# Optimization experiments

Hardware: AMD Instinct MI355X
Metric: run time of the kernel (lower is better)

The kernel has to match this reference:

```python
import jax, jax.numpy as jnp
import numpy as np

N_LOC = 20000
N_EXP = 200000
H = 64
E = 1500000
L = 400000


def setup_inputs() -> dict:
    key = jax.random.key(0)
    ks = jax.random.split(key, 24)
    f = jnp.float32
    w = lambda k, shp: jax.random.normal(k, shp, dtype=f) * 0.1
    # edges: ('location','of','experts'): src in [0,N_LOC), dst in [0,N_EXP)
    src = jax.random.randint(ks[0], (E,), 0, N_LOC)
    dst = jax.random.randint(ks[1], (E,), 0, N_EXP)
    edge_of = jnp.stack([src, dst])          # location -> experts
    edge_rev = jnp.stack([dst, src])         # experts -> location (ToUndirected)
    row = jax.random.randint(ks[2], (L,), 0, N_LOC)
    col = jax.random.randint(ks[3], (L,), 0, N_EXP)
    edge_label_index = jnp.stack([row, col])
    return dict(
        emb_loc=w(ks[4], (N_LOC, H)), emb_exp=w(ks[5], (N_EXP, H)),
        W1l_of=w(ks[6], (H, H)), b1_of=jnp.zeros((H,), f), W1r_of=w(ks[7], (H, H)),
        W1l_rev=w(ks[8], (H, H)), b1_rev=jnp.zeros((H,), f), W1r_rev=w(ks[9], (H, H)),
        W2l_of=w(ks[10], (H, H)), b2_of=jnp.zeros((H,), f), W2r_of=w(ks[11], (H, H)),
        W2l_rev=w(ks[12], (H, H)), b2_rev=jnp.zeros((H,), f), W2r_rev=w(ks[13], (H, H)),
        dW1=w(ks[14], (2 * H, H)), db1=jnp.zeros((H,), f),
        dW2=w(ks[15], (H, 1)), db2=jnp.zeros((1,), f),
        edge_of=edge_of, edge_rev=edge_rev, edge_label_index=edge_label_index,
    )


def _sage(x_src, x_dst, edge, Wl, b, Wr, n_dst):
    # PyG SAGEConv: lin_l(mean of neighbor msgs) + lin_r(x_dst); bias only in lin_l
    s, d = edge[0], edge[1]
    msg = x_src[s]                                   # [E, H] gather
    summed = jax.ops.segment_sum(msg, d, num_segments=n_dst)
    cnt = jax.ops.segment_sum(jnp.ones((edge.shape[1],), x_src.dtype), d, num_segments=n_dst)
    agg = summed / jnp.maximum(cnt, 1.0)[:, None]
    return agg @ Wl + b + x_dst @ Wr


def reference(emb_loc, emb_exp,
              W1l_of, b1_of, W1r_of, W1l_rev, b1_rev, W1r_rev,
              W2l_of, b2_of, W2r_of, W2l_rev, b2_rev, W2r_rev,
              dW1, db1, dW2, db2,
              edge_of, edge_rev, edge_label_index):
    # layer 1 (to_hetero: one conv per edge type; each dst type has one incoming type)
    z_exp = jax.nn.relu(_sage(emb_loc, emb_exp, edge_of, W1l_of, b1_of, W1r_of, N_EXP))
    z_loc = jax.nn.relu(_sage(emb_exp, emb_loc, edge_rev, W1l_rev, b1_rev, W1r_rev, N_LOC))
    # layer 2 (no relu)
    z_exp2 = _sage(z_loc, z_exp, edge_of, W2l_of, b2_of, W2r_of, N_EXP)
    z_loc2 = _sage(z_exp, z_loc, edge_rev, W2l_rev, b2_rev, W2r_rev, N_LOC)
    # EdgeDecoder: gather-concat-MLP
    row, col = edge_label_index[0], edge_label_index[1]
    z = jnp.concatenate([z_loc2[row], z_exp2[col]], axis=-1)  # [L, 2H]
    h = jax.nn.relu(z @ dW1 + db1)
    out = (h @ dW2 + db2).reshape(-1)
    return out
```

## Files before the change

kernel.cpp:

```cpp
#include <hip/hip_runtime.h>

#define H 64
#define NE 1500000
#define NLOC 20000
#define NEXP 200000
#define NL 400000
#define PAD_E 32
#define PAD_L 128
#define EPT 8
#define FILL_CHUNK 2048
#define NCHUNK ((NE + FILL_CHUNK - 1) / FILL_CHUNK)

#define WS_NEED 90546112ULL

typedef int vint4 __attribute__((ext_vector_type(4)));
typedef _Float16 f16x8 __attribute__((ext_vector_type(8)));
typedef float f32x4 __attribute__((ext_vector_type(4)));

__device__ __forceinline__ float bcastf(float v, int k) {
  return __int_as_float(__builtin_amdgcn_readlane(__float_as_int(v), k));
}
__device__ __forceinline__ int bcasti(int v, int k) {
  return __builtin_amdgcn_readlane(v, k);
}

__global__ __launch_bounds__(256) void fill_kernel(
    const int* __restrict__ src, const int* __restrict__ dst,
    int* __restrict__ cnt_loc, int* __restrict__ cnt_exp,
    int* __restrict__ nbr_loc, unsigned short* __restrict__ nbr_exp)
{
  const int p = blockIdx.x & 7;
  const int chunk = blockIdx.x >> 3;
  const long base = (long)chunk * FILL_CHUNK + threadIdx.x * EPT;
  if (base >= NE) return;
  vint4 s0 = __builtin_nontemporal_load((const vint4*)(src + base));
  vint4 s1 = __builtin_nontemporal_load((const vint4*)(src + base + 4));
  vint4 d0 = __builtin_nontemporal_load((const vint4*)(dst + base));
  vint4 d1 = __builtin_nontemporal_load((const vint4*)(dst + base + 4));
  int ss[EPT] = {s0.x, s0.y, s0.z, s0.w, s1.x, s1.y, s1.z, s1.w};
  int dd[EPT] = {d0.x, d0.y, d0.z, d0.w, d1.x, d1.y, d1.z, d1.w};
  const int elo = p * (NEXP / 8), ehi = elo + NEXP / 8;
  const int llo = p * (NLOC / 8), lhi = llo + NLOC / 8;
#pragma unroll
  for (int k = 0; k < EPT; k++) {
    const int d = dd[k];
    if (d >= elo && d < ehi) {
      int pos = atomicAdd(&cnt_exp[d], 1);
      if (pos < PAD_E) nbr_exp[d * PAD_E + pos] = (unsigned short)ss[k];
    }
  }
#pragma unroll
  for (int k = 0; k < EPT; k++) {
    const int s = ss[k];
    if (s >= llo && s < lhi) {
      int pos = atomicAdd(&cnt_loc[s], 1);
      if (pos < PAD_L) nbr_loc[s * PAD_L + pos] = dd[k];
    }
  }
}

__global__ __launch_bounds__(256) void fold_kernel(
    const float* __restrict__ W2r_of, const float* __restrict__ W2l_of,
    const float* __restrict__ W2l_rev, const float* __restrict__ W2r_rev,
    const float* __restrict__ dW1, const float* __restrict__ b2_of,
    const float* __restrict__ b2_rev,
    float* __restrict__ Wf_q, float* __restrict__ Wf_y2,
    float* __restrict__ Wf_t2, float* __restrict__ Wf_p,
    float* __restrict__ bf_q, float* __restrict__ bf_p)
{
  const int lane = threadIdx.x & 63;
  const int w = threadIdx.x >> 6;
  const float* dW1a = dW1;
  const float* dW1b = dW1 + H * H;
  if (blockIdx.x < 4) {
    const float* A; const float* B; float* C;
    switch (blockIdx.x) {
      case 0:  A = W2r_of;  B = dW1b; C = Wf_q;  break;
      case 1:  A = W2l_of;  B = dW1b; C = Wf_y2; break;
      case 2:  A = W2l_rev; B = dW1a; C = Wf_t2; break;
      default: A = W2r_rev; B = dW1a; C = Wf_p;  break;
    }
    float b[H];
#pragma unroll
    for (int k = 0; k < H; k++) b[k] = B[k * H + lane];
    for (int r = w * 16; r < w * 16 + 16; r++) {
      const float xv = A[r * H + lane];
      float a0 = 0.f, a1 = 0.f;
#pragma unroll
      for (int k = 0; k < H; k += 2) {
        a0 += bcastf(xv, k)     * b[k];
        a1 += bcastf(xv, k + 1) * b[k + 1];
      }
      C[r * H + lane] = a0 + a1;
    }
  } else if (w < 2) {
    const float* bv_src = (w == 0) ? b2_of : b2_rev;
    const float* B      = (w == 0) ? dW1b  : dW1a;
    float* o            = (w == 0) ? bf_q  : bf_p;
    float wk[H];
#pragma unroll
    for (int k = 0; k < H; k++) wk[k] = B[k * H + lane];
    const float bv = bv_src[lane];
    float a = 0.f;
#pragma unroll
    for (int k = 0; k < H; k++) a += bcastf(bv, k) * wk[k];
    o[lane] = a;
  }
}

__global__ __launch_bounds__(256, 4) void dense_linear_kernel(
    const float* __restrict__ x, _Float16* __restrict__ out16,
    const float* __restrict__ W, int n)
{
  const int lane = threadIdx.x & 63;
  const int gw = (blockIdx.x * 256 + threadIdx.x) >> 6;
  const int nw = (gridDim.x * 256) >> 6;
  float w[H];
#pragma unroll
  for (int k = 0; k < H; k++) w[k] = W[k * H + lane];
  for (int i = gw; i < n; i += nw) {
    const float xv = x[i * H + lane];
    float a0 = 0.f, a1 = 0.f;
#pragma unroll
    for (int k = 0; k < H; k += 2) {
      a0 += bcastf(xv, k)     * w[k];
      a1 += bcastf(xv, k + 1) * w[k + 1];
    }
    out16[i * H + lane] = (_Float16)(a0 + a1);
  }
}

__global__ __launch_bounds__(256, 4) void mfma_pass_kernel(
    const unsigned short* __restrict__ nbr, const int* __restrict__ cnt,
    const _Float16* __restrict__ y,
    const float* a32, const _Float16* a16,
    _Float16* out1, const float* __restrict__ W1,
    const float* __restrict__ bias, int relu,
    _Float16* out2, const float* __restrict__ W2)
{
  const int w = threadIdx.x >> 6;
  const int lane = threadIdx.x & 63;
  const int q = lane >> 4;
  const int cidx = lane & 15;
  const int rb = blockIdx.x * 16;

  __shared__ float Gs[16 * H];

  f16x8 b1lo, b1hi, b2lo, b2hi;
#pragma unroll
  for (int j = 0; j < 8; j++) {
    b1lo[j] = (_Float16)W1[(q * 8 + j) * H + w * 16 + cidx];
    b1hi[j] = (_Float16)W1[(32 + q * 8 + j) * H + w * 16 + cidx];
  }
  if (out2) {
#pragma unroll
    for (int j = 0; j < 8; j++) {
      b2lo[j] = (_Float16)W2[(q * 8 + j) * H + w * 16 + cidx];
      b2hi[j] = (_Float16)W2[(32 + q * 8 + j) * H + w * 16 + cidx];
    }
  }

  if (y) {
    for (int rr = 0; rr < 4; rr++) {
      const int i = rb + w * 4 + rr;
      const int c = cnt[i];
      const int cc = min(c, PAD_E);
      const unsigned short* nb = nbr + (long)i * PAD_E;
      float s0 = 0.f, s1 = 0.f, s2 = 0.f, s3 = 0.f;
      const int id = (lane < cc) ? (int)nb[lane] : 0;
      int k = 0;
      const int m4 = cc & ~3;
      for (; k < m4; k += 4) {
        const int i0 = bcasti(id, k), i1 = bcasti(id, k + 1),
                  i2 = bcasti(id, k + 2), i3 = bcasti(id, k + 3);
        s0 += (float)y[(long)i0 * H + lane];
        s1 += (float)y[(long)i1 * H + lane];
        s2 += (float)y[(long)i2 * H + lane];
        s3 += (float)y[(long)i3 * H + lane];
      }
      for (; k < cc; k++) s0 += (float)y[(long)bcasti(id, k) * H + lane];
      Gs[(w * 4 + rr) * H + lane] =
          ((s0 + s1) + (s2 + s3)) / fmaxf((float)c, 1.0f);
    }
  }

  f16x8 a0, a1;
  if (a16) {
    const _Float16* ar = a16 + (long)(rb + cidx) * H;
    a0 = *(const f16x8*)(ar + q * 8);
    a1 = *(const f16x8*)(ar + 32 + q * 8);
  } else {
    const float* ar = a32 + (long)(rb + cidx) * H;
#pragma unroll
    for (int j = 0; j < 8; j++) {
      a0[j] = (_Float16)ar[q * 8 + j];
      a1[j] = (_Float16)ar[32 + q * 8 + j];
    }
  }
  f32x4 acc1 = {0.f, 0.f, 0.f, 0.f};
  acc1 = __builtin_amdgcn_mfma_f32_16x16x32_f16(a0, b1lo, acc1, 0, 0, 0);
  acc1 = __builtin_amdgcn_mfma_f32_16x16x32_f16(a1, b1hi, acc1, 0, 0, 0);
  f32x4 acc2 = {0.f, 0.f, 0.f, 0.f};
  if (out2) {
    acc2 = __builtin_amdgcn_mfma_f32_16x16x32_f16(a0, b2lo, acc2, 0, 0, 0);
    acc2 = __builtin_amdgcn_mfma_f32_16x16x32_f16(a1, b2hi, acc2, 0, 0, 0);
  }

  const float bj = bias ? bias[w * 16 + cidx] : 0.f;
  __syncthreads();
#pragma unroll
  for (int reg = 0; reg < 4; reg++) {
    const int r = q * 4 + reg;
    float v = acc1[reg] + bj;
    if (y) v += Gs[r * H + w * 16 + cidx];
    if (relu) v = fmaxf(v, 0.f);
    out1[(long)(rb + r) * H + w * 16 + cidx] = (_Float16)v;
    if (out2)
      out2[(long)(rb + r) * H + w * 16 + cidx] = (_Float16)acc2[reg];
  }
}

__global__ __launch_bounds__(256, 4) void loc_gather_kernel(
    const int* __restrict__ nbr, const int* __restrict__ cnt,
    const _Float16* __restrict__ T, const float* __restrict__ x,
    float* __restrict__ out32, _Float16* __restrict__ out16,
    const float* __restrict__ Wr, const float* __restrict__ bias,
    int n, int relu)
{
  const int lane = threadIdx.x & 63;
  const int gw = (blockIdx.x * 256 + threadIdx.x) >> 6;
  const int nw = (gridDim.x * 256) >> 6;
  float wr[H];
#pragma unroll
  for (int k = 0; k < H; k++) wr[k] = Wr[k * H + lane];
  const float bj = bias[lane];
  for (int i = gw; i < n; i += nw) {
    const int c = cnt[i];
    const int cc = min(c, PAD_L);
    const int* nb = nbr + (long)i * PAD_L;
    float s0 = 0.f, s1 = 0.f, s2 = 0.f, s3 = 0.f;
    int e = 0;
    while (e < cc) {
      const int m = min(cc - e, 64);
      const int id = (lane < m) ? nb[e + lane] : 0;
      int k = 0;
      const int m4 = m & ~3;
      for (; k < m4; k += 4) {
        const int i0 = bcasti(id, k), i1 = bcasti(id, k + 1),
                  i2 = bcasti(id, k + 2), i3 = bcasti(id, k + 3);
        s0 += (float)T[(long)i0 * H + lane];
        s1 += (float)T[(long)i1 * H + lane];
        s2 += (float)T[(long)i2 * H + lane];
        s3 += (float)T[(long)i3 * H + lane];
      }
      for (; k < m; k++) s0 += (float)T[(long)bcasti(id, k) * H + lane];
      e += m;
    }
    const float agg = ((s0 + s1) + (s2 + s3)) / fmaxf((float)c, 1.0f);
    const float xv = x[i * H + lane];
    float a0 = 0.f, a1 = 0.f;
#pragma unroll
    for (int k = 0; k < H; k += 2) {
      a0 += bcastf(xv, k)     * wr[k];
      a1 += bcastf(xv, k + 1) * wr[k + 1];
    }
    float acc = agg + bj + a0 + a1;
    if (relu) acc = fmaxf(acc, 0.0f);
    if (out32) out32[i * H + lane] = acc;
    else       out16[i * H + lane] = (_Float16)acc;
  }
}

__global__ __launch_bounds__(256, 4) void edge_kernel(
    const int* __restrict__ row, const int* __restrict__ col,
    const _Float16* __restrict__ P, const _Float16* __restrict__ Q,
    const float* __restrict__ db1, const float* __restrict__ dW2,
    const float* __restrict__ db2, float* __restrict__ out)
{
  const int lane = threadIdx.x & 63;
  const int gw = (blockIdx.x * 256 + threadIdx.x) >> 6;
  const int nw = (gridDim.x * 256) >> 6;
  const float bj = db1[lane];
  const float w2 = dW2[lane];
  const float b2 = db2[0];
  for (int e = gw * 4; e < NL; e += nw * 4) {
    const int n4 = min(NL - e, 4);
    float h[4];
#pragma unroll
    for (int k = 0; k < 4; k++) {
      if (k < n4) {
        const int r = row[e + k], c = col[e + k];
        const float p = (float)P[(long)r * H + lane];
        const float q = (float)Q[(long)c * H + lane];
        h[k] = fmaxf(p + q + bj, 0.0f) * w2;
      } else h[k] = 0.f;
    }
#pragma unroll
    for (int off = 1; off < 64; off <<= 1) {
#pragma unroll
      for (int k = 0; k < 4; k++) h[k] += __shfl_xor(h[k], off);
    }
    if (lane == 0) {
#pragma unroll
      for (int k = 0; k < 4; k++)
        if (k < n4) out[e + k] = h[k] + b2;
    }
  }
}

extern "C" void kernel_launch(void* const* d_in, const int* in_sizes, int n_in,
                              void* d_out, int out_size, void* d_ws, size_t ws_size,
                              hipStream_t stream) {
  const float* emb_loc = (const float*)d_in[0];
  const float* emb_exp = (const float*)d_in[1];
  const float* W1l_of  = (const float*)d_in[2];
  const float* b1_of   = (const float*)d_in[3];
  const float* W1r_of  = (const float*)d_in[4];
  const float* W1l_rev = (const float*)d_in[5];
  const float* b1_rev  = (const float*)d_in[6];
  const float* W1r_rev = (const float*)d_in[7];
  const float* W2l_of  = (const float*)d_in[8];
  const float* b2_of   = (const float*)d_in[9];
  const float* W2r_of  = (const float*)d_in[10];
  const float* W2l_rev = (const float*)d_in[11];
  const float* b2_rev  = (const float*)d_in[12];
  const float* W2r_rev = (const float*)d_in[13];
  const float* dW1     = (const float*)d_in[14];
  const float* db1     = (const float*)d_in[15];
  const float* dW2     = (const float*)d_in[16];
  const float* db2     = (const float*)d_in[17];
  const int*   edge_of = (const int*)d_in[18];
  const int*   eli     = (const int*)d_in[20];

  const int* src = edge_of;
  const int* dst = edge_of + NE;
  const int* row = eli;
  const int* col = eli + NL;

  if (ws_size < WS_NEED) return;

  char* ws = (char*)d_ws;
  int*            cnt_loc = (int*)(ws);
  int*            cnt_exp = (int*)(ws + 80000);
  int*            nbr_loc = (int*)(ws + 880064);
  unsigned short* nbr_exp = (unsigned short*)(ws + 11120064);
  _Float16*       Ylh     = (_Float16*)(ws + 23920064);
  _Float16*       Y2fh    = (_Float16*)(ws + 26480064);
  float*          z_loc   = (float*)(ws + 29040064);
  _Float16*       PH      = (_Float16*)(ws + 34160064);
  _Float16*       ZE      = (_Float16*)(ws + 39280064);
  _Float16*       TH      = (_Float16*)(ws + 64880064);
  float*          Wf_q    = (float*)(ws + 90480064);
  float*          Wf_y2   = (float*)(ws + 90496448);
  float*          Wf_t2   = (float*)(ws + 90512832);
  float*          Wf_p    = (float*)(ws + 90529216);
  float*          bf_q    = (float*)(ws + 90545600);
  float*          bf_p    = (float*)(ws + 90545856);
  float*          out     = (float*)d_out;

  (void)hipMemsetAsync(ws, 0, 880000, stream);
  fill_kernel<<<NCHUNK * 8, 256, 0, stream>>>(src, dst, cnt_loc, cnt_exp,
                                              nbr_loc, nbr_exp);
  fold_kernel<<<5, 256, 0, stream>>>(W2r_of, W2l_of, W2l_rev, W2r_rev,
                                     dW1, b2_of, b2_rev,
                                     Wf_q, Wf_y2, Wf_t2, Wf_p, bf_q, bf_p);

  dense_linear_kernel<<<1280, 256, 0, stream>>>(emb_loc, Ylh, W1l_of, NLOC);
  mfma_pass_kernel<<<NEXP / 16, 256, 0, stream>>>(nbr_exp, cnt_exp, Ylh,
      emb_exp, (const _Float16*)nullptr, ZE, W1r_of, b1_of, 1, TH, W1l_rev);
  loc_gather_kernel<<<1250, 256, 0, stream>>>(nbr_loc, cnt_loc, TH,
      emb_loc, z_loc, (_Float16*)nullptr, W1r_rev, b1_rev, NLOC, 1);

  dense_linear_kernel<<<1280, 256, 0, stream>>>(z_loc, Y2fh, Wf_y2, NLOC);
  mfma_pass_kernel<<<NEXP / 16, 256, 0, stream>>>(nbr_exp, cnt_exp, Y2fh,
      (const float*)nullptr, ZE, ZE, Wf_q, bf_q, 0, TH, Wf_t2);
  loc_gather_kernel<<<1250, 256, 0, stream>>>(nbr_loc, cnt_loc, TH,
      z_loc, (float*)nullptr, PH, Wf_p, bf_p, NLOC, 0);

  edge_kernel<<<2048, 256, 0, stream>>>(row, col, PH, ZE,
                                        db1, dW2, db2, out);
}
```

Before: 600.8 us.

## Fuse fill, weight fold, and first dense linear into one persistent ticket kernel

Replaces three launches (CSR fill, weight folding, first dense linear) with one persistent kernel of 1536 blocks. The blocks pull work items from atomic ticket counters: fold tasks first, then dense-linear tiles, then fill chunks per partition, starting at the partition matching the block's XCD id. The goal is to remove launch gaps and tail idle time, and to keep each partition's atomics local to an XCD's L2. The cost is extra atomics on ticket counters, block-wide syncs per work item, and a larger memset to zero the tickets.

Measured after the change: 852.9 us. 1.42x slower.

```diff
diff --git a/kernel.cpp b/kernel.cpp
--- a/kernel.cpp
+++ b/kernel.cpp
@@ -10,6 +10,8 @@
 #define EPT 8
 #define FILL_CHUNK 2048
 #define NCHUNK ((NE + FILL_CHUNK - 1) / FILL_CHUNK)
+#define NDT ((NLOC + 63) / 64)
+#define NFILL 1536
 
 #define WS_NEED 90546112ULL
 
@@ -24,42 +26,13 @@
   return __builtin_amdgcn_readlane(v, k);
 }
 
-__global__ __launch_bounds__(256) void fill_kernel(
+__global__ __launch_bounds__(256) void mega_kernel(
     const int* __restrict__ src, const int* __restrict__ dst,
     int* __restrict__ cnt_loc, int* __restrict__ cnt_exp,
-    int* __restrict__ nbr_loc, unsigned short* __restrict__ nbr_exp)
-{
-  const int p = blockIdx.x & 7;
-  const int chunk = blockIdx.x >> 3;
-  const long base = (long)chunk * FILL_CHUNK + threadIdx.x * EPT;
-  if (base >= NE) return;
-  vint4 s0 = __builtin_nontemporal_load((const vint4*)(src + base));
-  vint4 s1 = __builtin_nontemporal_load((const vint4*)(src + base + 4));
-  vint4 d0 = __builtin_nontemporal_load((const vint4*)(dst + base));
-  vint4 d1 = __builtin_nontemporal_load((const vint4*)(dst + base + 4));
-  int ss[EPT] = {s0.x, s0.y, s0.z, s0.w, s1.x, s1.y, s1.z, s1.w};
-  int dd[EPT] = {d0.x, d0.y, d0.z, d0.w, d1.x, d1.y, d1.z, d1.w};
-  const int elo = p * (NEXP / 8), ehi = elo + NEXP / 8;
-  const int llo = p * (NLOC / 8), lhi = llo + NLOC / 8;
-#pragma unroll
-  for (int k = 0; k < EPT; k++) {
-    const int d = dd[k];
-    if (d >= elo && d < ehi) {
-      int pos = atomicAdd(&cnt_exp[d], 1);
-      if (pos < PAD_E) nbr_exp[d * PAD_E + pos] = (unsigned short)ss[k];
-    }
-  }
-#pragma unroll
-  for (int k = 0; k < EPT; k++) {
-    const int s = ss[k];
-    if (s >= llo && s < lhi) {
-      int pos = atomicAdd(&cnt_loc[s], 1);
-      if (pos < PAD_L) nbr_loc[s * PAD_L + pos] = dd[k];
-    }
-  }
-}
-
-__global__ __launch_bounds__(256) void fold_kernel(
+    int* __restrict__ nbr_loc, unsigned short* __restrict__ nbr_exp,
+    int* __restrict__ tickets,
+    const float* __restrict__ emb_loc, _Float16* __restrict__ Ylh,
+    const float* __restrict__ W1l_of,
     const float* __restrict__ W2r_of, const float* __restrict__ W2l_of,
     const float* __restrict__ W2l_rev, const float* __restrict__ W2r_rev,
     const float* __restrict__ dW1, const float* __restrict__ b2_of,
@@ -70,41 +43,131 @@
 {
   const int lane = threadIdx.x & 63;
   const int w = threadIdx.x >> 6;
-  const float* dW1a = dW1;
-  const float* dW1b = dW1 + H * H;
-  if (blockIdx.x < 4) {
-    const float* A; const float* B; float* C;
-    switch (blockIdx.x) {
-      case 0:  A = W2r_of;  B = dW1b; C = Wf_q;  break;
-      case 1:  A = W2l_of;  B = dW1b; C = Wf_y2; break;
-      case 2:  A = W2l_rev; B = dW1a; C = Wf_t2; break;
-      default: A = W2r_rev; B = dW1a; C = Wf_p;  break;
-    }
-    float b[H];
-#pragma unroll
-    for (int k = 0; k < H; k++) b[k] = B[k * H + lane];
-    for (int r = w * 16; r < w * 16 + 16; r++) {
-      const float xv = A[r * H + lane];
-      float a0 = 0.f, a1 = 0.f;
-#pragma unroll
-      for (int k = 0; k < H; k += 2) {
-        a0 += bcastf(xv, k)     * b[k];
-        a1 += bcastf(xv, k + 1) * b[k + 1];
-      }
-      C[r * H + lane] = a0 + a1;
-    }
-  } else if (w < 2) {
-    const float* bv_src = (w == 0) ? b2_of : b2_rev;
-    const float* B      = (w == 0) ? dW1b  : dW1a;
-    float* o            = (w == 0) ? bf_q  : bf_p;
-    float wk[H];
-#pragma unroll
-    for (int k = 0; k < H; k++) wk[k] = B[k * H + lane];
-    const float bv = bv_src[lane];
-    float a = 0.f;
-#pragma unroll
-    for (int k = 0; k < H; k++) a += bcastf(bv, k) * wk[k];
-    o[lane] = a;
+  __shared__ int s_t;
+
+  while (true) {
+    __syncthreads();
+    if (threadIdx.x == 0) {
+      int c = __hip_atomic_load(&tickets[9], __ATOMIC_RELAXED,
+                                __HIP_MEMORY_SCOPE_AGENT);
+      s_t = (c >= 5) ? 5 : atomicAdd(&tickets[9], 1);
+    }
+    __syncthreads();
+    const int t = s_t;
+    if (t >= 5) break;
+    const float* dW1a = dW1;
+    const float* dW1b = dW1 + H * H;
+    if (t < 4) {
+      const float* A; const float* B; float* C;
+      switch (t) {
+        case 0:  A = W2r_of;  B = dW1b; C = Wf_q;  break;
+        case 1:  A = W2l_of;  B = dW1b; C = Wf_y2; break;
+        case 2:  A = W2l_rev; B = dW1a; C = Wf_t2; break;
+        default: A = W2r_rev; B = dW1a; C = Wf_p;  break;
+      }
+      float b[H];
+#pragma unroll
+      for (int k = 0; k < H; k++) b[k] = B[k * H + lane];
+      for (int r = w * 16; r < w * 16 + 16; r++) {
+        const float xv = A[r * H + lane];
+        float a0 = 0.f, a1 = 0.f;
+#pragma unroll
+        for (int k = 0; k < H; k += 2) {
+          a0 += bcastf(xv, k)     * b[k];
+          a1 += bcastf(xv, k + 1) * b[k + 1];
+        }
+        C[r * H + lane] = a0 + a1;
+      }
+    } else if (w < 2) {
+      const float* bv_src = (w == 0) ? b2_of : b2_rev;
+      const float* B      = (w == 0) ? dW1b  : dW1a;
+      float* o            = (w == 0) ? bf_q  : bf_p;
+      float wk[H];
+#pragma unroll
+      for (int k = 0; k < H; k++) wk[k] = B[k * H + lane];
+      const float bv = bv_src[lane];
+      float a = 0.f;
+#pragma unroll
+      for (int k = 0; k < H; k++) a += bcastf(bv, k) * wk[k];
+      o[lane] = a;
+    }
+  }
+
+  {
+    bool wl = false;
+    float wreg[H];
+    while (true) {
+      __syncthreads();
+      if (threadIdx.x == 0) {
+        int c = __hip_atomic_load(&tickets[8], __ATOMIC_RELAXED,
+                                  __HIP_MEMORY_SCOPE_AGENT);
+        s_t = (c >= NDT) ? NDT : atomicAdd(&tickets[8], 1);
+      }
+      __syncthreads();
+      const int t = s_t;
+      if (t >= NDT) break;
+      if (!wl) {
+        wl = true;
+#pragma unroll
+        for (int k = 0; k < H; k++) wreg[k] = W1l_of[k * H + lane];
+      }
+      const int rbase = t * 64 + w * 16;
+      for (int rr = 0; rr < 16; rr++) {
+        const int r = rbase + rr;
+        if (r >= NLOC) break;
+        const float xv = emb_loc[r * H + lane];
+        float a0 = 0.f, a1 = 0.f;
+#pragma unroll
+        for (int k = 0; k < H; k += 2) {
+          a0 += bcastf(xv, k)     * wreg[k];
+          a1 += bcastf(xv, k + 1) * wreg[k + 1];
+        }
+        Ylh[(long)r * H + lane] = (_Float16)(a0 + a1);
+      }
+    }
+  }
+
+  const int xcd = (int)(__builtin_amdgcn_s_getreg(6164) & 7);
+  for (int pi = 0; pi < 8; pi++) {
+    const int p = (xcd + pi) & 7;
+    const int elo = p * (NEXP / 8), ehi = elo + NEXP / 8;
+    const int llo = p * (NLOC / 8), lhi = llo + NLOC / 8;
+    while (true) {
+      __syncthreads();
+      if (threadIdx.x == 0) {
+        int c = __hip_atomic_load(&tickets[p], __ATOMIC_RELAXED,
+                                  __HIP_MEMORY_SCOPE_AGENT);
+        s_t = (c >= NCHUNK) ? NCHUNK : atomicAdd(&tickets[p], 1);
+      }
+      __syncthreads();
+      const int chunk = s_t;
+      if (chunk >= NCHUNK) break;
+      const long base = (long)chunk * FILL_CHUNK + threadIdx.x * EPT;
+      if (base < NE) {
+        vint4 s0 = __builtin_nontemporal_load((const vint4*)(src + base));
+        vint4 s1 = __builtin_nontemporal_load((const vint4*)(src + base + 4));
+        vint4 d0 = __builtin_nontemporal_load((const vint4*)(dst + base));
+        vint4 d1 = __builtin_nontemporal_load((const vint4*)(dst + base + 4));
+        int ss[EPT] = {s0.x, s0.y, s0.z, s0.w, s1.x, s1.y, s1.z, s1.w};
+        int dd[EPT] = {d0.x, d0.y, d0.z, d0.w, d1.x, d1.y, d1.z, d1.w};
+#pragma unroll
+        for (int k = 0; k < EPT; k++) {
+          const int d = dd[k];
+          if (d >= elo && d < ehi) {
+            int pos = atomicAdd(&cnt_exp[d], 1);
+            if (pos < PAD_E) nbr_exp[d * PAD_E + pos] = (unsigned short)ss[k];
+          }
+        }
+#pragma unroll
+        for (int k = 0; k < EPT; k++) {
+          const int s = ss[k];
+          if (s >= llo && s < lhi) {
+            int pos = atomicAdd(&cnt_loc[s], 1);
+            if (pos < PAD_L) nbr_loc[s * PAD_L + pos] = dd[k];
+          }
+        }
+      }
+    }
   }
 }
 
@@ -342,6 +405,7 @@
   char* ws = (char*)d_ws;
   int*            cnt_loc = (int*)(ws);
   int*            cnt_exp = (int*)(ws + 80000);
+  int*            tickets = (int*)(ws + 880000);
   int*            nbr_loc = (int*)(ws + 880064);
   unsigned short* nbr_exp = (unsigned short*)(ws + 11120064);
   _Float16*       Ylh     = (_Float16*)(ws + 23920064);
@@ -358,14 +422,13 @@
   float*          bf_p    = (float*)(ws + 90545856);
   float*          out     = (float*)d_out;
 
-  (void)hipMemsetAsync(ws, 0, 880000, stream);
-  fill_kernel<<<NCHUNK * 8, 256, 0, stream>>>(src, dst, cnt_loc, cnt_exp,
-                                              nbr_loc, nbr_exp);
-  fold_kernel<<<5, 256, 0, stream>>>(W2r_of, W2l_of, W2l_rev, W2r_rev,
-                                     dW1, b2_of, b2_rev,
-                                     Wf_q, Wf_y2, Wf_t2, Wf_p, bf_q, bf_p);
-
-  dense_linear_kernel<<<1280, 256, 0, stream>>>(emb_loc, Ylh, W1l_of, NLOC);
+  (void)hipMemsetAsync(ws, 0, 880064, stream);
+
+  mega_kernel<<<NFILL, 256, 0, stream>>>(src, dst, cnt_loc, cnt_exp,
+      nbr_loc, nbr_exp, tickets, emb_loc, Ylh, W1l_of,
+      W2r_of, W2l_of, W2l_rev, W2r_rev, dW1, b2_of, b2_rev,
+      Wf_q, Wf_y2, Wf_t2, Wf_p, bf_q, bf_p);
+
   mfma_pass_kernel<<<NEXP / 16, 256, 0, stream>>>(nbr_exp, cnt_exp, Ylh,
       emb_exp, (const _Float16*)nullptr, ZE, W1r_of, b1_of, 1, TH, W1l_rev);
   loc_gather_kernel<<<1250, 256, 0, stream>>>(nbr_loc, cnt_loc, TH,
```

## Build padded adjacency via two-pass LDS binning instead of global atomics

Applied to the files above, without the earlier changes.

Replaces the global-atomic fill kernel with a two-stage build. First, edges are binned per block in shared memory into coarse destination buckets and appended to global queues. Then one block per bucket scatters its entries into LDS rows and writes the padded rows and counts out contiguously. Overflow edges go to a fallback queue that the fold kernel drains with global atomics. The aim is to cut scattered global atomics and random writes, at the cost of extra queue traffic, more kernels and a reused workspace region.

Result: faster. 527.1 us (-12.3%).

```diff
diff --git a/kernel.cpp b/kernel.cpp
--- a/kernel.cpp
+++ b/kernel.cpp
@@ -7,15 +7,27 @@
 #define NL 400000
 #define PAD_E 32
 #define PAD_L 128
-#define EPT 8
-#define FILL_CHUNK 2048
-#define NCHUNK ((NE + FILL_CHUNK - 1) / FILL_CHUNK)
+
+#define EB 896
+#define NBE 224
+#define LB 112
+#define NBL 179
+#define BIN_CHUNK 2048
+#define NBIN ((NE + BIN_CHUNK - 1) / BIN_CHUNK)
+#define EBSLOT 28
+#define LBSLOT 32
+#define ECAP 8192
+#define LCAP 10240
+#define FCAP 4096
 
 #define WS_NEED 90546112ULL
 
 typedef int vint4 __attribute__((ext_vector_type(4)));
 typedef _Float16 f16x8 __attribute__((ext_vector_type(8)));
 typedef float f32x4 __attribute__((ext_vector_type(4)));
+typedef unsigned int u32;
+typedef unsigned short u16;
+typedef unsigned long long u64;
 
 __device__ __forceinline__ float bcastf(float v, int k) {
   return __int_as_float(__builtin_amdgcn_readlane(__float_as_int(v), k));
@@ -24,38 +36,145 @@
   return __builtin_amdgcn_readlane(v, k);
 }
 
-__global__ __launch_bounds__(256) void fill_kernel(
+__global__ __launch_bounds__(256) void bin_kernel(
     const int* __restrict__ src, const int* __restrict__ dst,
-    int* __restrict__ cnt_loc, int* __restrict__ cnt_exp,
-    int* __restrict__ nbr_loc, unsigned short* __restrict__ nbr_exp)
-{
-  const int p = blockIdx.x & 7;
-  const int chunk = blockIdx.x >> 3;
-  const long base = (long)chunk * FILL_CHUNK + threadIdx.x * EPT;
-  if (base >= NE) return;
-  vint4 s0 = __builtin_nontemporal_load((const vint4*)(src + base));
-  vint4 s1 = __builtin_nontemporal_load((const vint4*)(src + base + 4));
-  vint4 d0 = __builtin_nontemporal_load((const vint4*)(dst + base));
-  vint4 d1 = __builtin_nontemporal_load((const vint4*)(dst + base + 4));
-  int ss[EPT] = {s0.x, s0.y, s0.z, s0.w, s1.x, s1.y, s1.z, s1.w};
-  int dd[EPT] = {d0.x, d0.y, d0.z, d0.w, d1.x, d1.y, d1.z, d1.w};
-  const int elo = p * (NEXP / 8), ehi = elo + NEXP / 8;
-  const int llo = p * (NLOC / 8), lhi = llo + NLOC / 8;
-#pragma unroll
-  for (int k = 0; k < EPT; k++) {
-    const int d = dd[k];
-    if (d >= elo && d < ehi) {
-      int pos = atomicAdd(&cnt_exp[d], 1);
-      if (pos < PAD_E) nbr_exp[d * PAD_E + pos] = (unsigned short)ss[k];
-    }
-  }
-#pragma unroll
-  for (int k = 0; k < EPT; k++) {
-    const int s = ss[k];
-    if (s >= llo && s < lhi) {
-      int pos = atomicAdd(&cnt_loc[s], 1);
-      if (pos < PAD_L) nbr_loc[s * PAD_L + pos] = dd[k];
-    }
+    u32* __restrict__ expQ, u32* __restrict__ locQ,
+    int* __restrict__ qcnt, int* __restrict__ flbk_cnt,
+    u64* __restrict__ flbkQ)
+{
+  __shared__ u32 eb[NBE * EBSLOT];
+  __shared__ u32 lb[NBL * LBSLOT];
+  __shared__ int ec[NBE], lc[NBL], ebase[NBE], lbase[NBL];
+
+  const int tid = threadIdx.x;
+  for (int i = tid; i < NBE; i += 256) ec[i] = 0;
+  for (int i = tid; i < NBL; i += 256) lc[i] = 0;
+  __syncthreads();
+
+  const long base = (long)blockIdx.x * BIN_CHUNK + tid * 8;
+  if (base < NE) {
+    vint4 s0 = __builtin_nontemporal_load((const vint4*)(src + base));
+    vint4 s1 = __builtin_nontemporal_load((const vint4*)(src + base + 4));
+    vint4 d0 = __builtin_nontemporal_load((const vint4*)(dst + base));
+    vint4 d1 = __builtin_nontemporal_load((const vint4*)(dst + base + 4));
+    int ss[8] = {s0.x, s0.y, s0.z, s0.w, s1.x, s1.y, s1.z, s1.w};
+    int dd[8] = {d0.x, d0.y, d0.z, d0.w, d1.x, d1.y, d1.z, d1.w};
+#pragma unroll
+    for (int k = 0; k < 8; k++) {
+      const u32 d = (u32)dd[k], s = (u32)ss[k];
+      {
+        const u32 b = d / (u32)EB;
+        const int pos = atomicAdd(&ec[b], 1);
+        if (pos < EBSLOT) {
+          eb[b * EBSLOT + pos] = ((d - b * EB) << 16) | s;
+        } else {
+          int fi = atomicAdd(flbk_cnt, 1);
+          if (fi < FCAP) flbkQ[fi] = ((u64)d << 32) | (u64)s;
+        }
+      }
+      {
+        const u32 b = s / (u32)LB;
+        const int pos = atomicAdd(&lc[b], 1);
+        if (pos < LBSLOT) {
+          lb[b * LBSLOT + pos] = ((s - b * LB) << 18) | d;
+        } else {
+          int fi = atomicAdd(flbk_cnt, 1);
+          if (fi < FCAP) flbkQ[fi] = (1ULL << 63) | ((u64)s << 32) | (u64)d;
+        }
+      }
+    }
+  }
+  __syncthreads();
+
+  for (int i = tid; i < NBE; i += 256) {
+    const int c = min(ec[i], EBSLOT);
+    ebase[i] = c ? atomicAdd(&qcnt[i], c) : 0;
+  }
+  for (int i = tid; i < NBL; i += 256) {
+    const int c = min(lc[i], LBSLOT);
+    lbase[i] = c ? atomicAdd(&qcnt[NBE + i], c) : 0;
+  }
+  __syncthreads();
+
+  const int wid = tid >> 6, ln = tid & 63;
+  for (int b = wid; b < NBE; b += 4) {
+    const int c = min(ec[b], EBSLOT);
+    if (ln < c) {
+      const int idx = ebase[b] + ln;
+      const u32 r = eb[b * EBSLOT + ln];
+      if (idx < ECAP) {
+        expQ[(long)b * ECAP + idx] = r;
+      } else {
+        int fi = atomicAdd(flbk_cnt, 1);
+        if (fi < FCAP)
+          flbkQ[fi] = ((u64)(b * EB + (r >> 16)) << 32) | (u64)(r & 0xFFFF);
+      }
+    }
+  }
+  for (int b = wid; b < NBL; b += 4) {
+    const int c = min(lc[b], LBSLOT);
+    if (ln < c) {
+      const int idx = lbase[b] + ln;
+      const u32 r = lb[b * LBSLOT + ln];
+      if (idx < LCAP) {
+        locQ[(long)b * LCAP + idx] = r;
+      } else {
+        int fi = atomicAdd(flbk_cnt, 1);
+        if (fi < FCAP)
+          flbkQ[fi] = (1ULL << 63) | ((u64)(b * LB + (r >> 18)) << 32) |
+                      (u64)(r & 0x3FFFF);
+      }
+    }
+  }
+}
+
+__global__ __launch_bounds__(256) void build_kernel(
+    const u32* __restrict__ expQ, const u32* __restrict__ locQ,
+    const int* __restrict__ qcnt,
+    u16* __restrict__ nbr_exp, int* __restrict__ nbr_loc,
+    int* __restrict__ cnt_exp, int* __restrict__ cnt_loc)
+{
+  __shared__ char ldsraw[60928];
+  const int tid = threadIdx.x;
+  if (blockIdx.x < NBE) {
+    const int b = blockIdx.x;
+    u16* rows = (u16*)ldsraw;
+    int* cnts = (int*)(ldsraw + 57344);
+    for (int i = tid; i < EB; i += 256) cnts[i] = 0;
+    __syncthreads();
+    const int n = min(qcnt[b], ECAP);
+    for (int i = tid; i < n; i += 256) {
+      const u32 r = expQ[(long)b * ECAP + i];
+      const int nl = (int)(r >> 16);
+      const int pos = atomicAdd(&cnts[nl], 1);
+      if (pos < PAD_E) rows[nl * PAD_E + pos] = (u16)(r & 0xFFFF);
+    }
+    __syncthreads();
+    const int node0 = b * EB;
+    const int nn = min(EB, NEXP - node0);
+    u32* grows = (u32*)(nbr_exp + (long)node0 * PAD_E);
+    const u32* lrows = (const u32*)rows;
+    for (int j = tid; j < nn * (PAD_E / 2); j += 256) grows[j] = lrows[j];
+    for (int i = tid; i < nn; i += 256) cnt_exp[node0 + i] = cnts[i];
+  } else {
+    const int b = blockIdx.x - NBE;
+    int* rows = (int*)ldsraw;
+    int* cnts = (int*)(ldsraw + 57344);
+    for (int i = tid; i < LB; i += 256) cnts[i] = 0;
+    __syncthreads();
+    const int n = min(qcnt[NBE + b], LCAP);
+    for (int i = tid; i < n; i += 256) {
+      const u32 r = locQ[(long)b * LCAP + i];
+      const int sl = (int)(r >> 18);
+      const int pos = atomicAdd(&cnts[sl], 1);
+      if (pos < PAD_L) rows[sl * PAD_L + pos] = (int)(r & 0x3FFFF);
+    }
+    __syncthreads();
+    const int node0 = b * LB;
+    const int nn = min(LB, NLOC - node0);
+    int* grows = nbr_loc + (long)node0 * PAD_L;
+    for (int j = tid; j < nn * PAD_L; j += 256) grows[j] = rows[j];
+    for (int i = tid; i < nn; i += 256) cnt_loc[node0 + i] = cnts[i];
   }
 }
 
@@ -66,7 +185,10 @@
     const float* __restrict__ b2_rev,
     float* __restrict__ Wf_q, float* __restrict__ Wf_y2,
     float* __restrict__ Wf_t2, float* __restrict__ Wf_p,
-    float* __restrict__ bf_q, float* __restrict__ bf_p)
+    float* __restrict__ bf_q, float* __restrict__ bf_p,
+    const int* __restrict__ flbk_cnt, const u64* __restrict__ flbkQ,
+    u16* __restrict__ nbr_exp, int* __restrict__ nbr_loc,
+    int* __restrict__ cnt_exp, int* __restrict__ cnt_loc)
 {
   const int lane = threadIdx.x & 63;
   const int w = threadIdx.x >> 6;
@@ -93,18 +215,34 @@
       }
       C[r * H + lane] = a0 + a1;
     }
-  } else if (w < 2) {
-    const float* bv_src = (w == 0) ? b2_of : b2_rev;
-    const float* B      = (w == 0) ? dW1b  : dW1a;
-    float* o            = (w == 0) ? bf_q  : bf_p;
-    float wk[H];
-#pragma unroll
-    for (int k = 0; k < H; k++) wk[k] = B[k * H + lane];
-    const float bv = bv_src[lane];
-    float a = 0.f;
-#pragma unroll
-    for (int k = 0; k < H; k++) a += bcastf(bv, k) * wk[k];
-    o[lane] = a;
+  } else if (blockIdx.x == 4) {
+    if (w < 2) {
+      const float* bv_src = (w == 0) ? b2_of : b2_rev;
+      const float* B      = (w == 0) ? dW1b  : dW1a;
+      float* o            = (w == 0) ? bf_q  : bf_p;
+      float wk[H];
+#pragma unroll
+      for (int k = 0; k < H; k++) wk[k] = B[k * H + lane];
+      const float bv = bv_src[lane];
+      float a = 0.f;
+#pragma unroll
+      for (int k = 0; k < H; k++) a += bcastf(bv, k) * wk[k];
+      o[lane] = a;
+    }
+  } else {
+    const int n = min(*flbk_cnt, FCAP);
+    for (int i = threadIdx.x; i < n; i += 256) {
+      const u64 rec = flbkQ[i];
+      const int node = (int)((rec >> 32) & 0x3FFFF);
+      const int val  = (int)(rec & 0x3FFFF);
+      if ((rec >> 63) == 0) {
+        int pos = atomicAdd(&cnt_exp[node], 1);
+        if (pos < PAD_E) nbr_exp[(long)node * PAD_E + pos] = (u16)val;
+      } else {
+        int pos = atomicAdd(&cnt_loc[node], 1);
+        if (pos < PAD_L) nbr_loc[(long)node * PAD_L + pos] = val;
+      }
+    }
   }
 }
 
@@ -350,6 +488,11 @@
   _Float16*       PH      = (_Float16*)(ws + 34160064);
   _Float16*       ZE      = (_Float16*)(ws + 39280064);
   _Float16*       TH      = (_Float16*)(ws + 64880064);
+  u32*            expQ    = (u32*)(ws + 64880064);
+  u32*            locQ    = (u32*)(ws + 72220096);
+  int*            qcnt    = (int*)(ws + 79551936);
+  int*            flbk    = (int*)(ws + 79553552);
+  u64*            flbkQ   = (u64*)(ws + 79554048);
   float*          Wf_q    = (float*)(ws + 90480064);
   float*          Wf_y2   = (float*)(ws + 90496448);
   float*          Wf_t2   = (float*)(ws + 90512832);
@@ -358,12 +501,16 @@
   float*          bf_p    = (float*)(ws + 90545856);
   float*          out     = (float*)d_out;
 
-  (void)hipMemsetAsync(ws, 0, 880000, stream);
-  fill_kernel<<<NCHUNK * 8, 256, 0, stream>>>(src, dst, cnt_loc, cnt_exp,
-                                              nbr_loc, nbr_exp);
-  fold_kernel<<<5, 256, 0, stream>>>(W2r_of, W2l_of, W2l_rev, W2r_rev,
+  (void)hipMemsetAsync(ws + 79551936, 0, 2048, stream);
+
+  bin_kernel<<<NBIN, 256, 0, stream>>>(src, dst, expQ, locQ, qcnt, flbk, flbkQ);
+  build_kernel<<<NBE + NBL, 256, 0, stream>>>(expQ, locQ, qcnt,
+      nbr_exp, nbr_loc, cnt_exp, cnt_loc);
+  fold_kernel<<<6, 256, 0, stream>>>(W2r_of, W2l_of, W2l_rev, W2r_rev,
                                      dW1, b2_of, b2_rev,
-                                     Wf_q, Wf_y2, Wf_t2, Wf_p, bf_q, bf_p);
+                                     Wf_q, Wf_y2, Wf_t2, Wf_p, bf_q, bf_p,
+                                     flbk, flbkQ, nbr_exp, nbr_loc,
+                                     cnt_exp, cnt_loc);
 
   dense_linear_kernel<<<1280, 256, 0, stream>>>(emb_loc, Ylh, W1l_of, NLOC);
   mfma_pass_kernel<<<NEXP / 16, 256, 0, stream>>>(nbr_exp, cnt_exp, Ylh,
```
